# Optimization experiments

Hardware: AMD Instinct MI355X
Metric: run time of the kernel (lower is better)

Reference implementation:

```python
import jax, jax.numpy as jnp
import numpy as np

B, T, C = 1, 2048, 1024
E = 32            # n_routed_experts
TOPK = 4
H = 512           # expert_hidden_size
HS = 1024         # shared hidden: round_up(2*512, 256)
ROUTE_SCALE = 1.0


def setup_inputs() -> dict:
    key = jax.random.key(0)
    ks = jax.random.split(key, 6)
    s = 0.02  # init scale for stable logits/activations
    return {
        "x": jax.random.normal(ks[0], (B, T, C), jnp.float32),
        "gate_w": jax.random.normal(ks[1], (C, E), jnp.float32) * s,
        "gate_bias": jnp.zeros((E,), jnp.float32),
        "shared_gate_w": jax.random.normal(ks[2], (C, 2 * HS), jnp.float32) * s,
        "shared_down_w": jax.random.normal(ks[3], (HS, C), jnp.float32) * s,
        "expert_gate_w": jax.random.normal(ks[4], (E, C, 2 * H), jnp.float32) * s,
        "expert_down_w": jax.random.normal(ks[5], (E, H, C), jnp.float32) * s,
    }


def _swiglu(x, gate_w, down_w):
    # torch: y, gate = chunk(gate_proj(x), 2); down(silu(gate) * y)
    u = x @ gate_w
    y, g = jnp.split(u, 2, axis=-1)
    return (jax.nn.silu(g) * y) @ down_w


def reference(x, gate_w, gate_bias, shared_gate_w, shared_down_w,
              expert_gate_w, expert_down_w):
    Bx, Tx, Cx = x.shape
    xf = x.reshape(-1, Cx)                     # (N, C)
    N = xf.shape[0]

    # shared expert (always active)
    shared = _swiglu(x, shared_gate_w, shared_down_w)   # (B, T, C)

    # sigmoid top-k gate with load-balance bias (bias only affects selection)
    scores = jax.nn.sigmoid(xf @ gate_w)                # (N, E)
    _, topk_idx = jax.lax.top_k(scores + gate_bias, TOPK)
    w = jnp.take_along_axis(scores, topk_idx, axis=-1)  # (N, K)
    w = w / jnp.sum(w, axis=-1, keepdims=True) * ROUTE_SCALE

    # dense combine weights: combine[n, e] = routing weight of expert e for token n (0 if unselected)
    combine = jnp.zeros((N, E), xf.dtype).at[jnp.arange(N)[:, None], topk_idx].add(w)

    # routed experts: masked dense evaluation (math identical to permute + grouped GEMM + scatter-combine)
    out = jnp.zeros_like(xf)
    for e in range(E):
        out = out + combine[:, e:e + 1] * _swiglu(xf, expert_gate_w[e], expert_down_w[e])

    return shared + out.reshape(Bx, Tx, Cx)
```

## Files before the change

### kernel.cpp

```cpp
#include <hip/hip_runtime.h>
#include <hip/hip_bf16.h>
#include <math.h>

#define N_TOK 2048
#define C_DIM 1024
#define E_NUM 32
#define TOPKK 4
#define H_EXP 512
#define HS_SH 1024
#define NSLOT (N_TOK * TOPKK)

typedef __attribute__((ext_vector_type(8))) short short8;
typedef __attribute__((ext_vector_type(4))) float f32x4;

__device__ __forceinline__ ushort f2b(float f) {
    __hip_bfloat16 h = __float2bfloat16(f);
    return *(ushort*)&h;
}
__device__ __forceinline__ float silu_f(float g) { return g / (1.f + __expf(-g)); }

__device__ __forceinline__ void glds16(const ushort* g, ushort* l) {
    __builtin_amdgcn_global_load_lds(
        (const __attribute__((address_space(1))) unsigned int*)g,
        (__attribute__((address_space(3))) unsigned int*)l, 16, 0, 0);
}

__device__ __forceinline__ void router_body(
    int n, int t, const float* __restrict__ x, const float* __restrict__ gate_w,
    const float* __restrict__ gate_bias, ushort* __restrict__ xb,
    int* __restrict__ topk_idx, float* __restrict__ topk_w, char* smem)
{
    float* xs = (float*)smem;
    float (*part)[E_NUM] = (float(*)[E_NUM])(smem + 4096);
    float* scores_s = (float*)(smem + 4096 + 1024);
    const float* xr = x + (size_t)n * C_DIM;
    {
        float4 v = ((const float4*)xr)[t];
        xs[t * 4 + 0] = v.x; xs[t * 4 + 1] = v.y;
        xs[t * 4 + 2] = v.z; xs[t * 4 + 3] = v.w;
        ushort4 o;
        o.x = f2b(v.x); o.y = f2b(v.y); o.z = f2b(v.z); o.w = f2b(v.w);
        ((ushort4*)(xb + (size_t)n * C_DIM))[t] = o;
    }
    __syncthreads();
    const int e = t & 31, cp = t >> 5;
    float s = 0.f;
#pragma unroll 4
    for (int c = cp * 128; c < cp * 128 + 128; ++c)
        s += xs[c] * gate_w[c * E_NUM + e];
    part[cp][e] = s;
    __syncthreads();
    if (t < E_NUM) {
        float tot = 0.f;
#pragma unroll
        for (int i = 0; i < 8; ++i) tot += part[i][t];
        scores_s[t] = 1.f / (1.f + expf(-tot));
    }
    __syncthreads();
    if (t < 64) {
        const int l = t;
        const float sc  = (l < E_NUM) ? scores_s[l] : -INFINITY;
        const float scb = (l < E_NUM) ? sc + gate_bias[l] : -INFINITY;
        bool used = false;
        int myidx[TOPKK]; float myw[TOPKK]; float wsum = 0.f;
#pragma unroll
        for (int k = 0; k < TOPKK; ++k) {
            float v = used ? -INFINITY : scb;
            float m = v;
#pragma unroll
            for (int d = 1; d < 64; d <<= 1) m = fmaxf(m, __shfl_xor(m, d));
            unsigned long long b = __ballot(v == m);
            const int pick = __ffsll((unsigned long long)b) - 1;
            if (l == pick) used = true;
            const float w = __shfl(sc, pick);
            myidx[k] = pick; myw[k] = w; wsum += w;
        }
        if (l == 0) {
            const float inv = 1.0f / wsum;
#pragma unroll
            for (int k = 0; k < TOPKK; ++k) {
                topk_idx[n * TOPKK + k] = myidx[k];
                topk_w[n * TOPKK + k] = myw[k] * inv;
            }
        }
    }
}

template<int K, int N, int PAIR_H>
__device__ __forceinline__ void transp_body(const float* __restrict__ in,
                                            ushort* __restrict__ out,
                                            int bx, int by, int bz, int t, char* smem)
{
    const float* inp = in + (size_t)bz * K * N;
    ushort* outp = out + (size_t)bz * K * N;
    ushort (*T)[136] = (ushort(*)[136])smem;
    const int k0 = by * 64, n0 = bx * 128;
    {
        const int row = t >> 5;
        const int c4  = (t & 31) * 4;
        float4 v[8];
#pragma unroll
        for (int i = 0; i < 8; ++i)
            v[i] = *(const float4*)(inp + (size_t)(k0 + row + i * 8) * N + n0 + c4);
#pragma unroll
        for (int i = 0; i < 8; ++i) {
            ushort4 o;
            o.x = f2b(v[i].x); o.y = f2b(v[i].y); o.z = f2b(v[i].z); o.w = f2b(v[i].w);
            *(ushort4*)&T[row + i * 8][c4] = o;
        }
    }
    __syncthreads();
    {
        const int g  = t >> 3;
        const int kg = t & 7;
#pragma unroll
        for (int p = 0; p < 4; ++p) {
            const int nn = p * 32 + g;
            const int gn = n0 + nn;
            int np;
            if (PAIR_H > 0)
                np = (gn < PAIR_H) ? ((gn >> 4) * 32 + (gn & 15))
                                   : (((gn - PAIR_H) >> 4) * 32 + 16 + ((gn - PAIR_H) & 15));
            else
                np = gn;
            short8 o;
#pragma unroll
            for (int j = 0; j < 8; ++j) o[j] = (short)T[kg * 8 + j][nn];
            *(short8*)(outp + (size_t)np * K + k0 + kg * 8) = o;
        }
    }
}

__global__ __launch_bounds__(256) void prep_mega(
    const float* __restrict__ x, const float* __restrict__ gw,
    const float* __restrict__ gb, const float* __restrict__ sgw,
    const float* __restrict__ sdw, const float* __restrict__ egw,
    const float* __restrict__ edw, ushort* __restrict__ xb,
    int* __restrict__ topk_idx, float* __restrict__ topk_w,
    ushort* __restrict__ sgw_t, ushort* __restrict__ sdw_t,
    ushort* __restrict__ egw_t, ushort* __restrict__ edw_t)
{
    __shared__ __align__(16) char smem[17408];
    const int b = blockIdx.x;
    const int t = threadIdx.x;
    if (b < 256) {
        transp_body<C_DIM, 2 * HS_SH, HS_SH>(sgw, sgw_t, b & 15, b >> 4, 0, t, smem);
    } else if (b < 384) {
        const int r = b - 256;
        transp_body<HS_SH, C_DIM, 0>(sdw, sdw_t, r & 7, r >> 3, 0, t, smem);
    } else if (b < 4480) {
        const int r = b - 384;
        transp_body<C_DIM, 2 * H_EXP, H_EXP>(egw, egw_t, r & 7, (r >> 3) & 15, r >> 7, t, smem);
    } else if (b < 6528) {
        const int r = b - 4480;
        transp_body<H_EXP, C_DIM, 0>(edw, edw_t, r & 7, (r >> 3) & 7, r >> 6, t, smem);
    } else {
        router_body(b - 6528, t, x, gw, gb, xb, topk_idx, topk_w, smem);
    }
}

__global__ __launch_bounds__(1024) void route_build(
    const int* __restrict__ topk_idx, const float* __restrict__ topk_w,
    int* __restrict__ offsets, int* __restrict__ perm_token,
    float* __restrict__ perm_w, int* __restrict__ inv_slot)
{
    __shared__ int cnt[E_NUM];
    __shared__ int off_s[E_NUM + 1];
    const int t = threadIdx.x;
    if (t < E_NUM) cnt[t] = 0;
    __syncthreads();
    int myidx[8];
#pragma unroll
    for (int j = 0; j < 8; ++j) {
        const int i = t * 8 + j;
        myidx[j] = topk_idx[i];
        atomicAdd(&cnt[myidx[j]], 1);
    }
    __syncthreads();
    if (t == 0) {
        int a = 0;
        for (int e2 = 0; e2 < E_NUM; ++e2) { off_s[e2] = a; a += cnt[e2]; }
        off_s[E_NUM] = a;
    }
    __syncthreads();
    if (t < E_NUM) cnt[t] = off_s[t];
    if (t <= E_NUM) offsets[t] = off_s[t];
    __syncthreads();
#pragma unroll
    for (int j = 0; j < 8; ++j) {
        const int i = t * 8 + j;
        const int pos = atomicAdd(&cnt[myidx[j]], 1);
        perm_token[pos] = i >> 2;
        perm_w[pos] = topk_w[i];
        inv_slot[i] = pos;
    }
}

template<int K, int NP, bool EXPERT>
__device__ __forceinline__ void swiglu_body(
    const ushort* __restrict__ Ab, const ushort* __restrict__ Bt,
    ushort* __restrict__ Out, const int* __restrict__ offsets,
    const int* __restrict__ perm_tok, int eidx, ushort* S)
{
    constexpr int H = NP / 2;
    int base = 0, cnt = N_TOK;
    const ushort* Bp = Bt;
    if (EXPERT) {
        base = offsets[eidx]; cnt = offsets[eidx + 1] - base;
        Bp = Bt + (size_t)eidx * NP * K;
    }
    const int n0 = blockIdx.x * 128;
    if (n0 >= NP) return;
    const int m0 = blockIdx.y * 128;
    if (m0 >= cnt) return;
    ushort* O = Out + (size_t)base * H;

    ushort* As = S;
    ushort* Bs = S + 128 * 64;

    const int t = threadIdx.x;
    const int lane = t & 63, wave = t >> 6;
    const int wr = wave >> 1, wc = wave & 1;
    const int quad = lane >> 4, l16 = lane & 15;
    const int srow = lane >> 3;
    const int schunk = (lane & 7) ^ srow;

    f32x4 acc[4][4];
#pragma unroll
    for (int i = 0; i < 4; ++i)
#pragma unroll
        for (int j = 0; j < 4; ++j) acc[i][j] = (f32x4){0.f, 0.f, 0.f, 0.f};

    const ushort* AgI[4];
#pragma unroll
    for (int i = 0; i < 4; ++i) {
        int ar = m0 + wave * 8 + srow + i * 32;
        if (EXPERT) {
            ar = ar < cnt ? ar : 0;
            AgI[i] = Ab + (size_t)perm_tok[base + ar] * K + schunk * 8;
        } else {
            AgI[i] = Ab + (size_t)(base + ar) * K + schunk * 8;
        }
    }
    const ushort* Bg = Bp + (size_t)(n0 + wave * 8 + srow) * K + schunk * 8;

    for (int k0 = 0; k0 < K; k0 += 64) {
        __syncthreads();
#pragma unroll
        for (int i = 0; i < 4; ++i) {
            glds16(AgI[i] + k0, As + (wave * 8 + i * 32) * 64);
            glds16(Bg + (size_t)(i * 32) * K + k0, Bs + (wave * 8 + i * 32) * 64);
        }
        __syncthreads();
#pragma unroll
        for (int ks = 0; ks < 2; ++ks) {
            const int coff = (((ks * 4 + quad) ^ (l16 & 7)) << 3);
            short8 af[4], bfr[4];
#pragma unroll
            for (int i = 0; i < 4; ++i) {
                af[i]  = *(const short8*)(As + (wr * 64 + i * 16 + l16) * 64 + coff);
                bfr[i] = *(const short8*)(Bs + (wc * 64 + i * 16 + l16) * 64 + coff);
            }
#pragma unroll
            for (int tm = 0; tm < 4; ++tm)
#pragma unroll
                for (int tn = 0; tn < 4; ++tn)
                    acc[tm][tn] = __builtin_amdgcn_mfma_f32_16x16x32_bf16(
                        af[tm], bfr[tn], acc[tm][tn], 0, 0, 0);
        }
    }

    __syncthreads();
#pragma unroll
    for (int tm = 0; tm < 4; ++tm)
#pragma unroll
        for (int p = 0; p < 2; ++p)
#pragma unroll
            for (int r = 0; r < 4; ++r) {
                const int ml = wr * 64 + tm * 16 + quad * 4 + r;
                const int hl = wc * 32 + p * 16 + l16;
                const float y = acc[tm][2 * p][r];
                const float g = acc[tm][2 * p + 1][r];
                S[ml * 72 + hl] = f2b(silu_f(g) * y);
            }
    __syncthreads();
#pragma unroll
    for (int i = 0; i < 4; ++i) {
        const int c = t + i * 256;
        const int row = c >> 3, col = (c & 7) * 8;
        if (m0 + row < cnt)
            *(float4*)(O + (size_t)(m0 + row) * H + (n0 >> 1) + col) =
                *(const float4*)(S + row * 72 + col);
    }
}

template<int K, bool EXPERT>
__device__ __forceinline__ void down_body(
    const ushort* __restrict__ Ab, const ushort* __restrict__ Bt,
    float* __restrict__ Out, const int* __restrict__ offsets,
    const float* __restrict__ perm_w, int eidx, ushort* S)
{
    int base = 0, cnt = N_TOK;
    const ushort* Bp = Bt;
    if (EXPERT) {
        base = offsets[eidx]; cnt = offsets[eidx + 1] - base;
        Bp = Bt + (size_t)eidx * C_DIM * K;
    }
    const int m0 = blockIdx.y * 128;
    if (m0 >= cnt) return;
    const int n0 = blockIdx.x * 128;
    const ushort* Ap = Ab + (size_t)base * K;

    ushort* As = S;
    ushort* Bs = S + 128 * 64;

    const int t = threadIdx.x;
    const int lane = t & 63, wave = t >> 6;
    const int wr = wave >> 1, wc = wave & 1;
    const int quad = lane >> 4, l16 = lane & 15;
    const int srow = lane >> 3;
    const int schunk = (lane & 7) ^ srow;

    f32x4 acc[4][4];
#pragma unroll
    for (int i = 0; i < 4; ++i)
#pragma unroll
        for (int j = 0; j < 4; ++j) acc[i][j] = (f32x4){0.f, 0.f, 0.f, 0.f};

    const ushort* Ag = Ap + (size_t)(m0 + wave * 8 + srow) * K + schunk * 8;
    const ushort* Bg = Bp + (size_t)(n0 + wave * 8 + srow) * K + schunk * 8;

    for (int k0 = 0; k0 < K; k0 += 64) {
        __syncthreads();
#pragma unroll
        for (int i = 0; i < 4; ++i) {
            glds16(Ag + (size_t)(i * 32) * K + k0, As + (wave * 8 + i * 32) * 64);
            glds16(Bg + (size_t)(i * 32) * K + k0, Bs + (wave * 8 + i * 32) * 64);
        }
        __syncthreads();
#pragma unroll
        for (int ks = 0; ks < 2; ++ks) {
            const int coff = (((ks * 4 + quad) ^ (l16 & 7)) << 3);
            short8 af[4], bfr[4];
#pragma unroll
            for (int i = 0; i < 4; ++i) {
                af[i]  = *(const short8*)(As + (wr * 64 + i * 16 + l16) * 64 + coff);
                bfr[i] = *(const short8*)(Bs + (wc * 64 + i * 16 + l16) * 64 + coff);
            }
#pragma unroll
            for (int tm = 0; tm < 4; ++tm)
#pragma unroll
                for (int tn = 0; tn < 4; ++tn)
                    acc[tm][tn] = __builtin_amdgcn_mfma_f32_16x16x32_bf16(
                        af[tm], bfr[tn], acc[tm][tn], 0, 0, 0);
        }
    }

#pragma unroll
    for (int tm = 0; tm < 4; ++tm)
#pragma unroll
        for (int r = 0; r < 4; ++r) {
            const int grow = m0 + wr * 64 + tm * 16 + quad * 4 + r;
            if (EXPERT) {
                if (grow < cnt) {
                    const float w = perm_w[base + grow];
#pragma unroll
                    for (int tn = 0; tn < 4; ++tn) {
                        const int col = n0 + wc * 64 + tn * 16 + l16;
                        Out[(size_t)(base + grow) * C_DIM + col] = w * acc[tm][tn][r];
                    }
                }
            } else {
#pragma unroll
                for (int tn = 0; tn < 4; ++tn) {
                    const int col = n0 + wc * 64 + tn * 16 + l16;
                    Out[(size_t)grow * C_DIM + col] = acc[tm][tn][r];
                }
            }
        }
}

__global__ __launch_bounds__(256, 3) void swiglu_fused(
    const ushort* __restrict__ xb, const ushort* __restrict__ sgw_t,
    const ushort* __restrict__ egw_t, ushort* __restrict__ Hs_b,
    ushort* __restrict__ He_b, const int* __restrict__ offsets,
    const int* __restrict__ perm_tok)
{
    __shared__ __align__(16) ushort S[2 * 128 * 64];
    const int z = blockIdx.z;
    if (z < E_NUM)
        swiglu_body<C_DIM, 2 * H_EXP, true>(xb, egw_t, He_b, offsets, perm_tok, z, S);
    else
        swiglu_body<C_DIM, 2 * HS_SH, false>(xb, sgw_t, Hs_b, nullptr, nullptr, 0, S);
}

__global__ __launch_bounds__(256, 3) void down_fused(
    const ushort* __restrict__ Hs_b, const ushort* __restrict__ He_b,
    const ushort* __restrict__ sdw_t, const ushort* __restrict__ edw_t,
    float* __restrict__ out, float* __restrict__ Ye,
    const int* __restrict__ offsets, const float* __restrict__ perm_w)
{
    __shared__ __align__(16) ushort S[2 * 128 * 64];
    const int z = blockIdx.z;
    if (z < E_NUM)
        down_body<H_EXP, true>(He_b, edw_t, Ye, offsets, perm_w, z, S);
    else
        down_body<HS_SH, false>(Hs_b, sdw_t, out, nullptr, nullptr, 0, S);
}

__global__ __launch_bounds__(256) void combine_kernel(
    const float* __restrict__ Ye, const int* __restrict__ inv_slot,
    float* __restrict__ Out)
{
    const int tok = blockIdx.x;
    __shared__ int s4[TOPKK];
    if (threadIdx.x < TOPKK) s4[threadIdx.x] = inv_slot[tok * TOPKK + threadIdx.x];
    __syncthreads();
    const int c = threadIdx.x * 4;
    float4 acc = *(const float4*)(Out + (size_t)tok * C_DIM + c);
#pragma unroll
    for (int k = 0; k < TOPKK; ++k) {
        float4 v = *(const float4*)(Ye + (size_t)s4[k] * C_DIM + c);
        acc.x += v.x; acc.y += v.y; acc.z += v.z; acc.w += v.w;
    }
    *(float4*)(Out + (size_t)tok * C_DIM + c) = acc;
}

extern "C" void kernel_launch(void* const* d_in, const int* in_sizes, int n_in,
                              void* d_out, int out_size, void* d_ws, size_t ws_size,
                              hipStream_t stream)
{
    const float* x   = (const float*)d_in[0];
    const float* gw  = (const float*)d_in[1];
    const float* gb  = (const float*)d_in[2];
    const float* sgw = (const float*)d_in[3];
    const float* sdw = (const float*)d_in[4];
    const float* egw = (const float*)d_in[5];
    const float* edw = (const float*)d_in[6];
    float* out = (float*)d_out;

    char* ws = (char*)d_ws;
    size_t off = 0;
    auto alloc = [&](size_t bytes) -> void* {
        void* p = ws + off;
        off = (off + bytes + 255) & ~(size_t)255;
        return p;
    };
    int*    topk_idx = (int*)   alloc((size_t)NSLOT * sizeof(int));
    float*  topk_w   = (float*) alloc((size_t)NSLOT * sizeof(float));
    int*    offsets  = (int*)   alloc((E_NUM + 1) * sizeof(int));
    int*    perm_tok = (int*)   alloc((size_t)NSLOT * sizeof(int));
    float*  perm_w   = (float*) alloc((size_t)NSLOT * sizeof(float));
    int*    inv_slot = (int*)   alloc((size_t)NSLOT * sizeof(int));
    ushort* xb       = (ushort*)alloc((size_t)N_TOK * C_DIM * 2);
    ushort* sgw_t    = (ushort*)alloc((size_t)C_DIM * 2 * HS_SH * 2);
    ushort* sdw_t    = (ushort*)alloc((size_t)HS_SH * C_DIM * 2);
    ushort* egw_t    = (ushort*)alloc((size_t)E_NUM * C_DIM * 2 * H_EXP * 2);
    ushort* edw_t    = (ushort*)alloc((size_t)E_NUM * H_EXP * C_DIM * 2);
    ushort* Hs_b     = (ushort*)alloc((size_t)N_TOK * HS_SH * 2);
    ushort* He_b     = (ushort*)alloc((size_t)(NSLOT + 128) * H_EXP * 2);
    float*  Ye       = (float*) alloc((size_t)(NSLOT + 128) * C_DIM * sizeof(float));
    (void)ws_size; (void)in_sizes; (void)n_in; (void)out_size;

    prep_mega<<<8576, 256, 0, stream>>>(x, gw, gb, sgw, sdw, egw, edw,
                                        xb, topk_idx, topk_w,
                                        sgw_t, sdw_t, egw_t, edw_t);
    route_build<<<1, 1024, 0, stream>>>(topk_idx, topk_w, offsets, perm_tok, perm_w, inv_slot);
    swiglu_fused<<<dim3(16, N_TOK / 128, E_NUM + 1), 256, 0, stream>>>(
        xb, sgw_t, egw_t, Hs_b, He_b, offsets, perm_tok);
    down_fused<<<dim3(C_DIM / 128, N_TOK / 128, E_NUM + 1), 256, 0, stream>>>(
        Hs_b, He_b, sdw_t, edw_t, out, Ye, offsets, perm_w);
    combine_kernel<<<N_TOK, 256, 0, stream>>>(Ye, inv_slot, out);
}
```

Baseline: 396.0 us.

## Move down-weight transposes into swiglu kernel and swizzle transpose LDS tile

Moves the fp32-to-bf16 transposition of the shared and expert down-projection weights out of the prep kernel and into extra z-slices of the swiglu kernel. Those blocks can then overlap with the gate GEMM work instead of delaying route_build and the swiglu launch. The transpose LDS tile also changes from padding to an XOR swizzle with a smaller row stride, aimed at cutting bank conflicts. The cost is that the swiglu grid grows and its GEMM blocks now share the GPU with memory-bound transpose blocks.

```diff
diff --git a/kernel.cpp b/kernel.cpp
--- a/kernel.cpp
+++ b/kernel.cpp
@@ -93,20 +93,21 @@
 {
     const float* inp = in + (size_t)bz * K * N;
     ushort* outp = out + (size_t)bz * K * N;
-    ushort (*T)[136] = (ushort(*)[136])smem;
+    ushort (*T)[132] = (ushort(*)[132])smem;
     const int k0 = by * 64, n0 = bx * 128;
     {
-        const int row = t >> 5;
-        const int c4  = (t & 31) * 4;
+        const int rr = t >> 5;
+        const int c4 = (t & 31) * 4;
         float4 v[8];
 #pragma unroll
         for (int i = 0; i < 8; ++i)
-            v[i] = *(const float4*)(inp + (size_t)(k0 + row + i * 8) * N + n0 + c4);
+            v[i] = *(const float4*)(inp + (size_t)(k0 + rr + i * 8) * N + n0 + c4);
 #pragma unroll
         for (int i = 0; i < 8; ++i) {
+            const int row = rr + i * 8;
             ushort4 o;
             o.x = f2b(v[i].x); o.y = f2b(v[i].y); o.z = f2b(v[i].z); o.w = f2b(v[i].w);
-            *(ushort4*)&T[row + i * 8][c4] = o;
+            *(ushort4*)&T[row][c4 ^ ((row >> 3) << 2)] = o;
         }
     }
     __syncthreads();
@@ -116,6 +117,7 @@
 #pragma unroll
         for (int p = 0; p < 4; ++p) {
             const int nn = p * 32 + g;
+            const int nsw = nn ^ (kg << 2);
             const int gn = n0 + nn;
             int np;
             if (PAIR_H > 0)
@@ -125,7 +127,7 @@
                 np = gn;
             short8 o;
 #pragma unroll
-            for (int j = 0; j < 8; ++j) o[j] = (short)T[kg * 8 + j][nn];
+            for (int j = 0; j < 8; ++j) o[j] = (short)T[kg * 8 + j][nsw];
             *(short8*)(outp + (size_t)np * K + k0 + kg * 8) = o;
         }
     }
@@ -134,28 +136,20 @@
 __global__ __launch_bounds__(256) void prep_mega(
     const float* __restrict__ x, const float* __restrict__ gw,
     const float* __restrict__ gb, const float* __restrict__ sgw,
-    const float* __restrict__ sdw, const float* __restrict__ egw,
-    const float* __restrict__ edw, ushort* __restrict__ xb,
+    const float* __restrict__ egw, ushort* __restrict__ xb,
     int* __restrict__ topk_idx, float* __restrict__ topk_w,
-    ushort* __restrict__ sgw_t, ushort* __restrict__ sdw_t,
-    ushort* __restrict__ egw_t, ushort* __restrict__ edw_t)
-{
-    __shared__ __align__(16) char smem[17408];
+    ushort* __restrict__ sgw_t, ushort* __restrict__ egw_t)
+{
+    __shared__ __align__(16) char smem[16896];
     const int b = blockIdx.x;
     const int t = threadIdx.x;
     if (b < 256) {
         transp_body<C_DIM, 2 * HS_SH, HS_SH>(sgw, sgw_t, b & 15, b >> 4, 0, t, smem);
-    } else if (b < 384) {
+    } else if (b < 4352) {
         const int r = b - 256;
-        transp_body<HS_SH, C_DIM, 0>(sdw, sdw_t, r & 7, r >> 3, 0, t, smem);
-    } else if (b < 4480) {
-        const int r = b - 384;
         transp_body<C_DIM, 2 * H_EXP, H_EXP>(egw, egw_t, r & 7, (r >> 3) & 15, r >> 7, t, smem);
-    } else if (b < 6528) {
-        const int r = b - 4480;
-        transp_body<H_EXP, C_DIM, 0>(edw, edw_t, r & 7, (r >> 3) & 7, r >> 6, t, smem);
     } else {
-        router_body(b - 6528, t, x, gw, gb, xb, topk_idx, topk_w, smem);
+        router_body(b - 4352, t, x, gw, gb, xb, topk_idx, topk_w, smem);
     }
 }
 
@@ -384,10 +378,24 @@
     const ushort* __restrict__ xb, const ushort* __restrict__ sgw_t,
     const ushort* __restrict__ egw_t, ushort* __restrict__ Hs_b,
     ushort* __restrict__ He_b, const int* __restrict__ offsets,
-    const int* __restrict__ perm_tok)
+    const int* __restrict__ perm_tok,
+    const float* __restrict__ sdw, const float* __restrict__ edw,
+    ushort* __restrict__ sdw_t, ushort* __restrict__ edw_t)
 {
     __shared__ __align__(16) ushort S[2 * 128 * 64];
     const int z = blockIdx.z;
+    if (z >= 33) {
+        const int flat = (z - 33) * 256 + blockIdx.y * 16 + blockIdx.x;
+        if (flat < 128) {
+            transp_body<HS_SH, C_DIM, 0>(sdw, sdw_t, flat & 7, flat >> 3, 0,
+                                         threadIdx.x, (char*)S);
+        } else if (flat < 2176) {
+            const int r = flat - 128;
+            transp_body<H_EXP, C_DIM, 0>(edw, edw_t, r & 7, (r >> 3) & 7, r >> 6,
+                                         threadIdx.x, (char*)S);
+        }
+        return;
+    }
     if (z < E_NUM)
         swiglu_body<C_DIM, 2 * H_EXP, true>(xb, egw_t, He_b, offsets, perm_tok, z, S);
     else
@@ -462,12 +470,11 @@
     float*  Ye       = (float*) alloc((size_t)(NSLOT + 128) * C_DIM * sizeof(float));
     (void)ws_size; (void)in_sizes; (void)n_in; (void)out_size;
 
-    prep_mega<<<8576, 256, 0, stream>>>(x, gw, gb, sgw, sdw, egw, edw,
-                                        xb, topk_idx, topk_w,
-                                        sgw_t, sdw_t, egw_t, edw_t);
+    prep_mega<<<6400, 256, 0, stream>>>(x, gw, gb, sgw, egw,
+                                        xb, topk_idx, topk_w, sgw_t, egw_t);
     route_build<<<1, 1024, 0, stream>>>(topk_idx, topk_w, offsets, perm_tok, perm_w, inv_slot);
-    swiglu_fused<<<dim3(16, N_TOK / 128, E_NUM + 1), 256, 0, stream>>>(
-        xb, sgw_t, egw_t, Hs_b, He_b, offsets, perm_tok);
+    swiglu_fused<<<dim3(16, N_TOK / 128, 42), 256, 0, stream>>>(
+        xb, sgw_t, egw_t, Hs_b, He_b, offsets, perm_tok, sdw, edw, sdw_t, edw_t);
     down_fused<<<dim3(C_DIM / 128, N_TOK / 128, E_NUM + 1), 256, 0, stream>>>(
         Hs_b, He_b, sdw_t, edw_t, out, Ye, offsets, perm_w);
     combine_kernel<<<N_TOK, 256, 0, stream>>>(Ye, inv_slot, out);
```

Measured after the change: 379.6 us. 1.04x faster.
